# Kernel tuning notes

Measured on AMD Instinct MI355X. Metric: run time of the kernel, lower is better.

## Reference

```python
import jax, jax.numpy as jnp
import numpy as np

N = 100000      # num nodes
E = 1600000     # num edges (before self-loops)
F_IN = 500      # num_features
H1, C1 = 8, 8   # heads, hidden_dim (layer 1, concat)
H2, C2 = 1, 16  # output_heads, num_classes (layer 2, mean)
NEG_SLOPE = 0.2


def setup_inputs() -> dict:
    key = jax.random.key(0)
    ks = jax.random.split(key, 10)
    x = jax.random.normal(ks[0], (N, F_IN), dtype=jnp.float32)
    edge_index = jax.random.randint(ks[1], (2, E), 0, N, dtype=jnp.int64)
    s = 0.05
    W1 = jax.random.normal(ks[2], (F_IN, H1 * C1), dtype=jnp.float32) * s
    a_src1 = jax.random.normal(ks[3], (H1, C1), dtype=jnp.float32) * s
    a_dst1 = jax.random.normal(ks[4], (H1, C1), dtype=jnp.float32) * s
    b1 = jnp.zeros((H1 * C1,), dtype=jnp.float32)
    W2 = jax.random.normal(ks[5], (H1 * C1, H2 * C2), dtype=jnp.float32) * s
    a_src2 = jax.random.normal(ks[6], (H2, C2), dtype=jnp.float32) * s
    a_dst2 = jax.random.normal(ks[7], (H2, C2), dtype=jnp.float32) * s
    b2 = jnp.zeros((C2,), dtype=jnp.float32)
    return {"x": x, "edge_index": edge_index, "W1": W1, "a_src1": a_src1,
            "a_dst1": a_dst1, "b1": b1, "W2": W2, "a_src2": a_src2,
            "a_dst2": a_dst2, "b2": b2}


def _gat_conv(x, src, dst, W, a_src, a_dst, bias, heads, out_c, concat):
    n = x.shape[0]
    xw = (x @ W).reshape(n, heads, out_c)                      # [N,H,C]
    # per-node attention halves, gathered per edge -> logits [E,H]
    s_src = jnp.einsum('nhc,hc->nh', xw, a_src)
    s_dst = jnp.einsum('nhc,hc->nh', xw, a_dst)
    e = s_src[src] + s_dst[dst]
    e = jnp.where(e > 0, e, NEG_SLOPE * e)                     # leaky_relu
    # segment softmax over incoming edges of each target node
    m = jax.ops.segment_max(e, dst, num_segments=n)            # [N,H]
    m = jnp.where(jnp.isfinite(m), m, 0.0)
    p = jnp.exp(e - m[dst])                                    # [E,H]
    denom = jax.ops.segment_sum(p, dst, num_segments=n)        # [N,H]
    alpha = p / denom[dst]                                     # [E,H]
    # scatter-aggregate weighted messages
    out = jax.ops.segment_sum(alpha[:, :, None] * xw[src], dst,
                              num_segments=n)                  # [N,H,C]
    if concat:
        out = out.reshape(n, heads * out_c)
    else:
        out = out.mean(axis=1)
    return out + bias


def reference(x, edge_index, W1, a_src1, a_dst1, b1, W2, a_src2, a_dst2, b2):
    # PyG GATConv adds self-loops by default
    loops = jnp.arange(N, dtype=edge_index.dtype)
    src = jnp.concatenate([edge_index[0], loops])
    dst = jnp.concatenate([edge_index[1], loops])
    # eval mode: dropout is identity
    h = _gat_conv(x, src, dst, W1, a_src1, a_dst1, b1, H1, C1, True)
    h = jax.nn.elu(h)
    h = _gat_conv(h, src, dst, W2, a_src2, a_dst2, b2, H2, C2, False)
    return jax.nn.log_softmax(h, axis=1)
```

## Files before the change

kernel.cpp:

```cpp
#include <hip/hip_runtime.h>
#include <math.h>

#define NEGS 0.2f
#define BSH 9
#define TS 4096

typedef __attribute__((ext_vector_type(8))) short bf16x8;
typedef __attribute__((ext_vector_type(8))) unsigned short u16x8;
typedef __attribute__((ext_vector_type(4))) float f32x4;

__device__ __forceinline__ unsigned short f2bf(float f) {
  unsigned u = __float_as_uint(f);
  u += 0x7fffu + ((u >> 16) & 1);
  return (unsigned short)(u >> 16);
}
__device__ __forceinline__ float bf2f(unsigned short u) {
  return __uint_as_float((unsigned)u << 16);
}

__global__ void k_wcvt(const float* __restrict__ W1, unsigned short* __restrict__ Wb,
                       int K, int Kp) {
  int t = blockIdx.x * blockDim.x + threadIdx.x;
  if (t >= Kp * 64) return;
  int kg = t >> 6;
  int c = t & 63;
  float f = (kg < K) ? W1[(size_t)kg * 64 + c] : 0.f;
  size_t off = ((size_t)((kg >> 5) * 4 + ((kg >> 3) & 3)) * 512) + c * 8 + (kg & 7);
  Wb[off] = f2bf(f);
}

__global__ __launch_bounds__(256) void k_gemm1m(const float* __restrict__ A,
                                                const unsigned short* __restrict__ Wb,
                                                unsigned short* __restrict__ C,
                                                int M, int K, int nck) {
  const int tid = threadIdx.x;
  const int lane = tid & 63;
  const int w = tid >> 6;
  const int r15 = lane & 15;
  const int kgrp = lane >> 4;
  const int bm = blockIdx.x * 64;

  const int row = bm + w * 16 + r15;
  const float* Ar = A + (size_t)(row < M ? row : (M - 1)) * K;

  f32x4 acc[4] = {};

  for (int ck = 0; ck < nck; ++ck) {
#pragma unroll
    for (int ks = 0; ks < 2; ++ks) {
      const int k0 = ck * 64 + ks * 32 + kgrp * 8;
      bf16x8 af;
      if (ck < nck - 1) {
        const float4* g = (const float4*)(Ar + k0);
        float4 f0 = g[0], f1 = g[1];
        unsigned pk[4];
        pk[0] = (unsigned)f2bf(f0.x) | ((unsigned)f2bf(f0.y) << 16);
        pk[1] = (unsigned)f2bf(f0.z) | ((unsigned)f2bf(f0.w) << 16);
        pk[2] = (unsigned)f2bf(f1.x) | ((unsigned)f2bf(f1.y) << 16);
        pk[3] = (unsigned)f2bf(f1.z) | ((unsigned)f2bf(f1.w) << 16);
        af = *(bf16x8*)pk;
      } else {
        float f[8];
#pragma unroll
        for (int j = 0; j < 8; ++j) {
          int kk = k0 + j;
          f[j] = (kk < K) ? Ar[kk] : 0.f;
        }
        unsigned pk[4];
#pragma unroll
        for (int j = 0; j < 4; ++j)
          pk[j] = (unsigned)f2bf(f[2 * j]) | ((unsigned)f2bf(f[2 * j + 1]) << 16);
        af = *(bf16x8*)pk;
      }
      const unsigned short* bb =
          Wb + ((size_t)((ck * 2 + ks) * 4 + kgrp) * 512) + r15 * 8;
      bf16x8 bf[4];
#pragma unroll
      for (int nc = 0; nc < 4; ++nc)
        bf[nc] = *(const bf16x8*)(bb + nc * 128);
#pragma unroll
      for (int nc = 0; nc < 4; ++nc)
        acc[nc] = __builtin_amdgcn_mfma_f32_16x16x32_bf16(af, bf[nc], acc[nc], 0, 0, 0);
    }
  }
  const int rg4 = kgrp * 4;
#pragma unroll
  for (int nc = 0; nc < 4; ++nc) {
    int row0 = bm + w * 16 + rg4;
    int colg = nc * 16 + r15;
#pragma unroll
    for (int j = 0; j < 4; ++j) {
      int grow = row0 + j;
      if (grow < M) C[(size_t)grow * 64 + colg] = f2bf(acc[nc][j]);
    }
  }
}

__global__ __launch_bounds__(256) void k_thist(const int* __restrict__ ei,
                                               int* __restrict__ hist,
                                               int E, int NB) {
  __shared__ int lh[256];
  const int t = threadIdx.x;
  lh[t] = 0;
  __syncthreads();
  const int e0 = blockIdx.x * TS;
#pragma unroll
  for (int j = 0; j < TS / 256; ++j) {
    int e = e0 + j * 256 + t;
    if (e < E) atomicAdd(&lh[ei[E + e] >> BSH], 1);
  }
  __syncthreads();
  if (t < NB) hist[blockIdx.x * NB + t] = lh[t];
}

__global__ __launch_bounds__(256) void k_bscan1(const int* __restrict__ hist,
                                                int* __restrict__ off_rel,
                                                int* __restrict__ total,
                                                int NT, int NB) {
  __shared__ int sh[256];
  const int t = threadIdx.x;
  const int b = blockIdx.x;
  int t0 = 2 * t, t1 = 2 * t + 1;
  int v0 = (t0 < NT) ? hist[t0 * NB + b] : 0;
  int v1 = (t1 < NT) ? hist[t1 * NB + b] : 0;
  int ps = v0 + v1;
  sh[t] = ps;
  __syncthreads();
  for (int off = 1; off < 256; off <<= 1) {
    int v = (t >= off) ? sh[t - off] : 0;
    __syncthreads();
    sh[t] += v;
    __syncthreads();
  }
  int excl = sh[t] - ps;
  if (t0 < NT) off_rel[t0 * NB + b] = excl;
  if (t1 < NT) off_rel[t1 * NB + b] = excl + v0;
  if (t == 255) total[b] = sh[255];
}

__global__ __launch_bounds__(256) void k_pscatter(const int* __restrict__ ei,
                                                  const int* __restrict__ off_rel,
                                                  const int* __restrict__ total,
                                                  unsigned* __restrict__ pairs,
                                                  int E, int NB) {
  __shared__ int cur[256];
  __shared__ int sb[256];
  const int t = threadIdx.x;
  int v = (t < NB) ? total[t] : 0;
  sb[t] = v;
  __syncthreads();
  for (int off = 1; off < 256; off <<= 1) {
    int x = (t >= off) ? sb[t - off] : 0;
    __syncthreads();
    sb[t] += x;
    __syncthreads();
  }
  if (t < NB) cur[t] = (sb[t] - v) + off_rel[blockIdx.x * NB + t];
  __syncthreads();
  const int e0 = blockIdx.x * TS;
#pragma unroll
  for (int j = 0; j < TS / 256; ++j) {
    int e = e0 + j * 256 + t;
    if (e < E) {
      int s = ei[e], d = ei[E + e];
      int pos = atomicAdd(&cur[d >> BSH], 1);
      pairs[pos] = ((unsigned)(d & ((1 << BSH) - 1)) << 23) | (unsigned)s;
    }
  }
}

__global__ __launch_bounds__(256) void k_bcsr(const unsigned* __restrict__ pairs,
                                              const int* __restrict__ total,
                                              int* __restrict__ rowptr,
                                              int* __restrict__ col,
                                              int Nn, int E, int NB) {
  __shared__ int cnt[512];
  __shared__ int cu[512];
  __shared__ int sh[256];
  __shared__ int P0, P1;
  const int t = threadIdx.x;
  const int b = blockIdx.x;
  const int d0 = b << BSH;
  const int dn = min(1 << BSH, Nn - d0);
  {
    int v = (t < NB) ? total[t] : 0;
    sh[t] = v;
    __syncthreads();
    for (int off = 1; off < 256; off <<= 1) {
      int x = (t >= off) ? sh[t - off] : 0;
      __syncthreads();
      sh[t] += x;
      __syncthreads();
    }
    if (t == b) { P0 = sh[t] - v; P1 = sh[t]; }
    __syncthreads();
  }
  const int p0 = P0, p1 = P1;
  const int rpb = p0 + d0;
  cnt[2 * t] = (2 * t < dn) ? 1 : 0;
  cnt[2 * t + 1] = (2 * t + 1 < dn) ? 1 : 0;
  __syncthreads();
  for (int i = p0 + t; i < p1; i += 256) atomicAdd(&cnt[pairs[i] >> 23], 1);
  __syncthreads();
  int a0 = cnt[2 * t], a1 = cnt[2 * t + 1];
  int ps = a0 + a1;
  sh[t] = ps;
  __syncthreads();
  for (int off = 1; off < 256; off <<= 1) {
    int v = (t >= off) ? sh[t - off] : 0;
    __syncthreads();
    sh[t] += v;
    __syncthreads();
  }
  int excl = sh[t] - ps;
#pragma unroll
  for (int u = 0; u < 2; ++u) {
    int i = 2 * t + u;
    int ex = (u == 0) ? excl : excl + a0;
    if (i < dn) {
      rowptr[d0 + i] = rpb + ex;
      col[rpb + ex] = d0 + i;
      cu[i] = ex + 1;
    }
  }
  if (b == NB - 1 && t == 0) rowptr[Nn] = E + Nn;
  __syncthreads();
  for (int i = p0 + t; i < p1; i += 256) {
    unsigned p = pairs[i];
    int pos = atomicAdd(&cu[p >> 23], 1);
    col[rpb + pos] = (int)(p & 0x7fffffu);
  }
}

__global__ void k_prep1(const unsigned short* __restrict__ xwb,
                        const float* __restrict__ asr,
                        const float* __restrict__ adt,
                        float* __restrict__ ssrc, float* __restrict__ sdst,
                        int Nn) {
  int idx = blockIdx.x * blockDim.x + threadIdx.x;
  if (idx >= Nn * 8) return;
  int h = idx & 7;
  const uint4 v = *(const uint4*)(xwb + (size_t)(idx >> 3) * 64 + h * 8);
  float f[8];
  f[0] = __uint_as_float(v.x << 16); f[1] = __uint_as_float(v.x & 0xffff0000u);
  f[2] = __uint_as_float(v.y << 16); f[3] = __uint_as_float(v.y & 0xffff0000u);
  f[4] = __uint_as_float(v.z << 16); f[5] = __uint_as_float(v.z & 0xffff0000u);
  f[6] = __uint_as_float(v.w << 16); f[7] = __uint_as_float(v.w & 0xffff0000u);
  float ss = 0.f, sd = 0.f;
#pragma unroll
  for (int c = 0; c < 8; ++c) {
    ss += f[c] * asr[h * 8 + c];
    sd += f[c] * adt[h * 8 + c];
  }
  ssrc[idx] = ss;
  sdst[idx] = sd;
}

__global__ __launch_bounds__(256) void k_agg1(const int* __restrict__ rowptr,
                                              const int* __restrict__ col,
                                              const float* __restrict__ ssrc,
                                              const float* __restrict__ sdst,
                                              const unsigned short* __restrict__ xwb,
                                              const float* __restrict__ b1,
                                              float* __restrict__ h1, int Nn) {
  int wid = (blockIdx.x * 256 + threadIdx.x) >> 6;
  if (wid >= Nn) return;
  int lane = threadIdx.x & 63;
  int slot = lane >> 3;
  int chg = lane & 7;
  float sd = sdst[wid * 8 + chg];
  int start = rowptr[wid], end = rowptr[wid + 1];
  float den = 0.f;
  float acc[8] = {};
  for (int it = start; it < end; it += 8) {
    int idx = it + slot;
    bool ok = idx < end;
    int s = col[ok ? idx : start];
    u16x8 pv = *(const u16x8*)(xwb + (size_t)s * 64 + chg * 8);
    float v = ssrc[s * 8 + chg] + sd;
    v = v > 0.f ? v : NEGS * v;
    float p = ok ? __expf(v) : 0.f;
    den += p;
#pragma unroll
    for (int j = 0; j < 8; ++j) acc[j] = fmaf(p, bf2f(pv[j]), acc[j]);
  }
#pragma unroll
  for (int off = 8; off < 64; off <<= 1) {
    den += __shfl_xor(den, off);
#pragma unroll
    for (int j = 0; j < 8; ++j) acc[j] += __shfl_xor(acc[j], off);
  }
  if (slot == 0) {
    float inv = 1.f / den;
    float o[8];
#pragma unroll
    for (int j = 0; j < 8; ++j) {
      float v = acc[j] * inv + b1[chg * 8 + j];
      o[j] = v > 0.f ? v : (__expf(v) - 1.f);
    }
    float* dst = h1 + (size_t)wid * 64 + chg * 8;
#pragma unroll
    for (int j = 0; j < 8; ++j) dst[j] = o[j];
  }
}

__global__ __launch_bounds__(256) void k_gemm2p(const float* __restrict__ h1,
                                                const float* __restrict__ W2,
                                                const float* __restrict__ asr,
                                                const float* __restrict__ adt,
                                                float* __restrict__ xw2,
                                                float* __restrict__ ssrc,
                                                float* __restrict__ sdst, int Nn) {
  __shared__ float w[64 * 16];
  int tid = threadIdx.x;
  for (int i = tid; i < 1024; i += 256) w[i] = W2[i];
  __syncthreads();
  int idx = blockIdx.x * 256 + tid;
  if (idx >= Nn * 16) return;
  int n = idx >> 4, c = idx & 15;
  const float* hr = h1 + (size_t)n * 64;
  float acc = 0.f;
#pragma unroll 8
  for (int k = 0; k < 64; ++k) acc += hr[k] * w[k * 16 + c];
  xw2[idx] = acc;
  float ssv = acc * asr[c], sdv = acc * adt[c];
#pragma unroll
  for (int off = 1; off < 16; off <<= 1) {
    ssv += __shfl_xor(ssv, off);
    sdv += __shfl_xor(sdv, off);
  }
  if (c == 0) { ssrc[n] = ssv; sdst[n] = sdv; }
}

__global__ __launch_bounds__(256) void k_agg2(const int* __restrict__ rowptr,
                                              const int* __restrict__ col,
                                              const float* __restrict__ ssrc,
                                              const float* __restrict__ sdst,
                                              const float* __restrict__ xw2,
                                              const float* __restrict__ b2,
                                              float* __restrict__ out, int Nn) {
  int wid = (blockIdx.x * 256 + threadIdx.x) >> 6;
  if (wid >= Nn) return;
  int lane = threadIdx.x & 63;
  int slot = lane >> 4, c = lane & 15;
  float sd = sdst[wid];
  int start = rowptr[wid], end = rowptr[wid + 1];
  float den = 0.f, acc = 0.f;
  int i = start + slot;
  for (; i + 4 < end; i += 8) {
    int s0 = col[i], s1 = col[i + 4];
    float w0 = xw2[(size_t)s0 * 16 + c];
    float w1 = xw2[(size_t)s1 * 16 + c];
    float v0 = ssrc[s0] + sd; v0 = v0 > 0.f ? v0 : NEGS * v0;
    float v1 = ssrc[s1] + sd; v1 = v1 > 0.f ? v1 : NEGS * v1;
    float p0 = __expf(v0), p1 = __expf(v1);
    den += p0 + p1;
    acc = fmaf(p0, w0, acc);
    acc = fmaf(p1, w1, acc);
  }
  if (i < end) {
    int s = col[i];
    float v = ssrc[s] + sd;
    v = v > 0.f ? v : NEGS * v;
    float p = __expf(v);
    den += p;
    acc = fmaf(p, xw2[(size_t)s * 16 + c], acc);
  }
  den += __shfl_xor(den, 16);
  den += __shfl_xor(den, 32);
  acc += __shfl_xor(acc, 16);
  acc += __shfl_xor(acc, 32);
  float o = acc / den + b2[c];
  float mx = o;
#pragma unroll
  for (int off = 1; off < 16; off <<= 1) mx = fmaxf(mx, __shfl_xor(mx, off));
  float ex = __expf(o - mx);
  float ssum = ex;
#pragma unroll
  for (int off = 1; off < 16; off <<= 1) ssum += __shfl_xor(ssum, off);
  float r = o - mx - __logf(ssum);
  if (slot == 0) out[(size_t)wid * 16 + c] = r;
}

extern "C" void kernel_launch(void* const* d_in, const int* in_sizes, int n_in,
                              void* d_out, int out_size, void* d_ws, size_t ws_size,
                              hipStream_t stream) {
  const float* x      = (const float*)d_in[0];
  const int* ei       = (const int*)d_in[1];
  const float* W1     = (const float*)d_in[2];
  const float* a_src1 = (const float*)d_in[3];
  const float* a_dst1 = (const float*)d_in[4];
  const float* b1     = (const float*)d_in[5];
  const float* W2     = (const float*)d_in[6];
  const float* a_src2 = (const float*)d_in[7];
  const float* a_dst2 = (const float*)d_in[8];
  const float* b2     = (const float*)d_in[9];

  const int F    = in_sizes[2] / 64;
  const int Nn   = in_sizes[0] / F;
  const int E    = in_sizes[1] / 2;
  const int Etot = E + Nn;
  const int nck  = (F + 63) >> 6;
  const int Kp   = nck * 64;
  const int NB   = (Nn + (1 << BSH) - 1) >> BSH;
  const int NT   = (E + TS - 1) / TS;

  float* ws = (float*)d_ws;
  unsigned short* xwb = (unsigned short*)ws;
  float* h1     = ws + (size_t)Nn * 32;
  float* ssrc1  = h1 + (size_t)Nn * 64;
  float* sdst1  = ssrc1 + (size_t)Nn * 8;
  int* rowptr   = (int*)(sdst1 + (size_t)Nn * 8);
  int* col      = rowptr + Nn + 1;
  unsigned short* Wb = (unsigned short*)(col + ((Etot + 7) & ~7));
  int* hist     = (int*)ws;
  int* off_rel  = hist + (size_t)NT * NB;
  int* total    = off_rel + (size_t)NT * NB;
  unsigned* pairs = (unsigned*)h1;
  float* xw2    = ws;
  float* ssrc2  = xw2 + (size_t)Nn * 16;
  float* sdst2  = ssrc2 + Nn;
  float* out2   = (float*)d_out;

  dim3 blk(256);

  k_thist<<<dim3(NT), blk, 0, stream>>>(ei, hist, E, NB);
  k_bscan1<<<dim3(NB), blk, 0, stream>>>(hist, off_rel, total, NT, NB);
  k_pscatter<<<dim3(NT), blk, 0, stream>>>(ei, off_rel, total, pairs, E, NB);
  k_bcsr<<<dim3(NB), blk, 0, stream>>>(pairs, total, rowptr, col, Nn, E, NB);

  k_wcvt<<<dim3((Kp * 64 + 255) / 256), blk, 0, stream>>>(W1, Wb, F, Kp);
  k_gemm1m<<<dim3((Nn + 63) / 64), blk, 0, stream>>>(x, Wb, xwb, Nn, F, nck);
  k_prep1<<<dim3((Nn * 8 + 255) / 256), blk, 0, stream>>>(
      xwb, a_src1, a_dst1, ssrc1, sdst1, Nn);
  k_agg1<<<dim3((Nn * 64 + 255) / 256), blk, 0, stream>>>(
      rowptr, col, ssrc1, sdst1, xwb, b1, h1, Nn);

  k_gemm2p<<<dim3((Nn * 16 + 255) / 256), blk, 0, stream>>>(
      h1, W2, a_src2, a_dst2, xw2, ssrc2, sdst2, Nn);
  k_agg2<<<dim3((Nn * 64 + 255) / 256), blk, 0, stream>>>(
      rowptr, col, ssrc2, sdst2, xw2, b2, out2, Nn);
}
```

Measured before the change: 239.0 us.

## Co-schedule CSR build with layer-1 GEMM and fuse attention scores into GEMM

Merges the W1 conversion with the edge histogram into one launch. It then splits the layer-1 GEMM row blocks into thirds, each launched alongside a latency-bound CSR-building stage (scan, scatter, bucket CSR), so the small graph-prep kernels overlap with matrix work. The per-node attention scores are computed inside the GEMM epilogue with shuffles, which removes the separate prep kernel and its re-read of xw. Layer-2 features are stored as bf16 to halve gather traffic in agg2, at some precision cost. Workspace for hist is moved so it no longer aliases the GEMM output.

```diff
diff --git a/kernel.cpp b/kernel.cpp
--- a/kernel.cpp
+++ b/kernel.cpp
@@ -1,4 +1,5 @@
 #include <hip/hip_runtime.h>
+#include <hip/hip_bf16.h>
 #include <math.h>
 
 #define NEGS 0.2f
@@ -10,116 +11,53 @@
 typedef __attribute__((ext_vector_type(4))) float f32x4;
 
 __device__ __forceinline__ unsigned short f2bf(float f) {
-  unsigned u = __float_as_uint(f);
-  u += 0x7fffu + ((u >> 16) & 1);
-  return (unsigned short)(u >> 16);
+  __hip_bfloat16 h = __float2bfloat16(f);
+  unsigned short u;
+  __builtin_memcpy(&u, &h, 2);
+  return u;
 }
 __device__ __forceinline__ float bf2f(unsigned short u) {
   return __uint_as_float((unsigned)u << 16);
 }
-
-__global__ void k_wcvt(const float* __restrict__ W1, unsigned short* __restrict__ Wb,
-                       int K, int Kp) {
-  int t = blockIdx.x * blockDim.x + threadIdx.x;
+__device__ __forceinline__ unsigned packbf(float lo, float hi) {
+  return (unsigned)f2bf(lo) | ((unsigned)f2bf(hi) << 16);
+}
+
+
+__device__ __forceinline__ void dev_wcvt(const float* __restrict__ W1,
+                                         unsigned short* __restrict__ Wb,
+                                         int K, int Kp, int blk) {
+  int t = blk * 256 + threadIdx.x;
   if (t >= Kp * 64) return;
-  int kg = t >> 6;
-  int c = t & 63;
+  int kg = t >> 6, c = t & 63;
   float f = (kg < K) ? W1[(size_t)kg * 64 + c] : 0.f;
   size_t off = ((size_t)((kg >> 5) * 4 + ((kg >> 3) & 3)) * 512) + c * 8 + (kg & 7);
   Wb[off] = f2bf(f);
 }
 
-__global__ __launch_bounds__(256) void k_gemm1m(const float* __restrict__ A,
-                                                const unsigned short* __restrict__ Wb,
-                                                unsigned short* __restrict__ C,
-                                                int M, int K, int nck) {
-  const int tid = threadIdx.x;
-  const int lane = tid & 63;
-  const int w = tid >> 6;
-  const int r15 = lane & 15;
-  const int kgrp = lane >> 4;
-  const int bm = blockIdx.x * 64;
-
-  const int row = bm + w * 16 + r15;
-  const float* Ar = A + (size_t)(row < M ? row : (M - 1)) * K;
-
-  f32x4 acc[4] = {};
-
-  for (int ck = 0; ck < nck; ++ck) {
-#pragma unroll
-    for (int ks = 0; ks < 2; ++ks) {
-      const int k0 = ck * 64 + ks * 32 + kgrp * 8;
-      bf16x8 af;
-      if (ck < nck - 1) {
-        const float4* g = (const float4*)(Ar + k0);
-        float4 f0 = g[0], f1 = g[1];
-        unsigned pk[4];
-        pk[0] = (unsigned)f2bf(f0.x) | ((unsigned)f2bf(f0.y) << 16);
-        pk[1] = (unsigned)f2bf(f0.z) | ((unsigned)f2bf(f0.w) << 16);
-        pk[2] = (unsigned)f2bf(f1.x) | ((unsigned)f2bf(f1.y) << 16);
-        pk[3] = (unsigned)f2bf(f1.z) | ((unsigned)f2bf(f1.w) << 16);
-        af = *(bf16x8*)pk;
-      } else {
-        float f[8];
-#pragma unroll
-        for (int j = 0; j < 8; ++j) {
-          int kk = k0 + j;
-          f[j] = (kk < K) ? Ar[kk] : 0.f;
-        }
-        unsigned pk[4];
-#pragma unroll
-        for (int j = 0; j < 4; ++j)
-          pk[j] = (unsigned)f2bf(f[2 * j]) | ((unsigned)f2bf(f[2 * j + 1]) << 16);
-        af = *(bf16x8*)pk;
-      }
-      const unsigned short* bb =
-          Wb + ((size_t)((ck * 2 + ks) * 4 + kgrp) * 512) + r15 * 8;
-      bf16x8 bf[4];
-#pragma unroll
-      for (int nc = 0; nc < 4; ++nc)
-        bf[nc] = *(const bf16x8*)(bb + nc * 128);
-#pragma unroll
-      for (int nc = 0; nc < 4; ++nc)
-        acc[nc] = __builtin_amdgcn_mfma_f32_16x16x32_bf16(af, bf[nc], acc[nc], 0, 0, 0);
-    }
-  }
-  const int rg4 = kgrp * 4;
-#pragma unroll
-  for (int nc = 0; nc < 4; ++nc) {
-    int row0 = bm + w * 16 + rg4;
-    int colg = nc * 16 + r15;
-#pragma unroll
-    for (int j = 0; j < 4; ++j) {
-      int grow = row0 + j;
-      if (grow < M) C[(size_t)grow * 64 + colg] = f2bf(acc[nc][j]);
-    }
-  }
-}
-
-__global__ __launch_bounds__(256) void k_thist(const int* __restrict__ ei,
-                                               int* __restrict__ hist,
-                                               int E, int NB) {
+__device__ __forceinline__ void dev_thist(const int* __restrict__ ei,
+                                          int* __restrict__ hist,
+                                          int E, int NB, int tile) {
   __shared__ int lh[256];
   const int t = threadIdx.x;
   lh[t] = 0;
   __syncthreads();
-  const int e0 = blockIdx.x * TS;
+  const int e0 = tile * TS;
 #pragma unroll
   for (int j = 0; j < TS / 256; ++j) {
     int e = e0 + j * 256 + t;
     if (e < E) atomicAdd(&lh[ei[E + e] >> BSH], 1);
   }
   __syncthreads();
-  if (t < NB) hist[blockIdx.x * NB + t] = lh[t];
-}
-
-__global__ __launch_bounds__(256) void k_bscan1(const int* __restrict__ hist,
-                                                int* __restrict__ off_rel,
-                                                int* __restrict__ total,
-                                                int NT, int NB) {
+  if (t < NB) hist[tile * NB + t] = lh[t];
+}
+
+__device__ __forceinline__ void dev_bscan1(const int* __restrict__ hist,
+                                           int* __restrict__ off_rel,
+                                           int* __restrict__ total,
+                                           int NT, int NB, int b) {
   __shared__ int sh[256];
   const int t = threadIdx.x;
-  const int b = blockIdx.x;
   int t0 = 2 * t, t1 = 2 * t + 1;
   int v0 = (t0 < NT) ? hist[t0 * NB + b] : 0;
   int v1 = (t1 < NT) ? hist[t1 * NB + b] : 0;
@@ -138,11 +76,11 @@
   if (t == 255) total[b] = sh[255];
 }
 
-__global__ __launch_bounds__(256) void k_pscatter(const int* __restrict__ ei,
-                                                  const int* __restrict__ off_rel,
-                                                  const int* __restrict__ total,
-                                                  unsigned* __restrict__ pairs,
-                                                  int E, int NB) {
+__device__ __forceinline__ void dev_pscatter(const int* __restrict__ ei,
+                                             const int* __restrict__ off_rel,
+                                             const int* __restrict__ total,
+                                             unsigned* __restrict__ pairs,
+                                             int E, int NB, int tile) {
   __shared__ int cur[256];
   __shared__ int sb[256];
   const int t = threadIdx.x;
@@ -155,9 +93,9 @@
     sb[t] += x;
     __syncthreads();
   }
-  if (t < NB) cur[t] = (sb[t] - v) + off_rel[blockIdx.x * NB + t];
-  __syncthreads();
-  const int e0 = blockIdx.x * TS;
+  if (t < NB) cur[t] = (sb[t] - v) + off_rel[tile * NB + t];
+  __syncthreads();
+  const int e0 = tile * TS;
 #pragma unroll
   for (int j = 0; j < TS / 256; ++j) {
     int e = e0 + j * 256 + t;
@@ -169,17 +107,16 @@
   }
 }
 
-__global__ __launch_bounds__(256) void k_bcsr(const unsigned* __restrict__ pairs,
-                                              const int* __restrict__ total,
-                                              int* __restrict__ rowptr,
-                                              int* __restrict__ col,
-                                              int Nn, int E, int NB) {
-  __shared__ int cnt[512];
-  __shared__ int cu[512];
+__device__ __forceinline__ void dev_bcsr(const unsigned* __restrict__ pairs,
+                                         const int* __restrict__ total,
+                                         int* __restrict__ rowptr,
+                                         int* __restrict__ col,
+                                         int Nn, int E, int NB, int b) {
+  __shared__ int cnt[1 << BSH];
+  __shared__ int cu[1 << BSH];
   __shared__ int sh[256];
   __shared__ int P0, P1;
   const int t = threadIdx.x;
-  const int b = blockIdx.x;
   const int d0 = b << BSH;
   const int dn = min(1 << BSH, Nn - d0);
   {
@@ -232,28 +169,147 @@
   }
 }
 
-__global__ void k_prep1(const unsigned short* __restrict__ xwb,
-                        const float* __restrict__ asr,
-                        const float* __restrict__ adt,
-                        float* __restrict__ ssrc, float* __restrict__ sdst,
-                        int Nn) {
-  int idx = blockIdx.x * blockDim.x + threadIdx.x;
-  if (idx >= Nn * 8) return;
-  int h = idx & 7;
-  const uint4 v = *(const uint4*)(xwb + (size_t)(idx >> 3) * 64 + h * 8);
-  float f[8];
-  f[0] = __uint_as_float(v.x << 16); f[1] = __uint_as_float(v.x & 0xffff0000u);
-  f[2] = __uint_as_float(v.y << 16); f[3] = __uint_as_float(v.y & 0xffff0000u);
-  f[4] = __uint_as_float(v.z << 16); f[5] = __uint_as_float(v.z & 0xffff0000u);
-  f[6] = __uint_as_float(v.w << 16); f[7] = __uint_as_float(v.w & 0xffff0000u);
-  float ss = 0.f, sd = 0.f;
-#pragma unroll
-  for (int c = 0; c < 8; ++c) {
-    ss += f[c] * asr[h * 8 + c];
-    sd += f[c] * adt[h * 8 + c];
-  }
-  ssrc[idx] = ss;
-  sdst[idx] = sd;
+__device__ __forceinline__ void dev_gemm(const float* __restrict__ A,
+                                         const unsigned short* __restrict__ Wb,
+                                         unsigned short* __restrict__ C,
+                                         const float* __restrict__ a1s,
+                                         const float* __restrict__ a1d,
+                                         float* __restrict__ ssrc,
+                                         float* __restrict__ sdst,
+                                         int M, int K, int nck, int rowblk) {
+  const int tid = threadIdx.x;
+  const int lane = tid & 63;
+  const int w = tid >> 6;
+  const int r15 = lane & 15;
+  const int kgrp = lane >> 4;
+  const int bm = rowblk * 64;
+  const int row = bm + w * 16 + r15;
+  const float* Ar = A + (size_t)(row < M ? row : (M - 1)) * K;
+
+  f32x4 acc[4] = {};
+
+  for (int ck = 0; ck < nck; ++ck) {
+#pragma unroll
+    for (int ks = 0; ks < 2; ++ks) {
+      const int k0 = ck * 64 + ks * 32 + kgrp * 8;
+      bf16x8 af;
+      if (ck < nck - 1) {
+        const float4* g = (const float4*)(Ar + k0);
+        float4 f0 = g[0], f1 = g[1];
+        unsigned pk[4] = { packbf(f0.x, f0.y), packbf(f0.z, f0.w),
+                           packbf(f1.x, f1.y), packbf(f1.z, f1.w) };
+        af = *(bf16x8*)pk;
+      } else {
+        float f[8];
+#pragma unroll
+        for (int j = 0; j < 8; ++j) {
+          int kk = k0 + j;
+          f[j] = (kk < K) ? Ar[kk] : 0.f;
+        }
+        unsigned pk[4];
+#pragma unroll
+        for (int j = 0; j < 4; ++j) pk[j] = packbf(f[2 * j], f[2 * j + 1]);
+        af = *(bf16x8*)pk;
+      }
+      const unsigned short* bb =
+          Wb + ((size_t)((ck * 2 + ks) * 4 + kgrp) * 512) + r15 * 8;
+      bf16x8 bf4[4];
+#pragma unroll
+      for (int nc = 0; nc < 4; ++nc)
+        bf4[nc] = *(const bf16x8*)(bb + nc * 128);
+#pragma unroll
+      for (int nc = 0; nc < 4; ++nc)
+        acc[nc] = __builtin_amdgcn_mfma_f32_16x16x32_bf16(af, bf4[nc], acc[nc], 0, 0, 0);
+    }
+  }
+  float av[4], dv[4];
+#pragma unroll
+  for (int nc = 0; nc < 4; ++nc) {
+    av[nc] = a1s[nc * 16 + r15];
+    dv[nc] = a1d[nc * 16 + r15];
+  }
+#pragma unroll
+  for (int j = 0; j < 4; ++j) {
+    int grow = bm + w * 16 + kgrp * 4 + j;
+    bool liv = grow < M;
+#pragma unroll
+    for (int nc = 0; nc < 4; ++nc) {
+      if (liv) C[(size_t)grow * 64 + nc * 16 + r15] = f2bf(acc[nc][j]);
+      float ss = acc[nc][j] * av[nc];
+      float sd = acc[nc][j] * dv[nc];
+      ss += __shfl_xor(ss, 1); ss += __shfl_xor(ss, 2); ss += __shfl_xor(ss, 4);
+      sd += __shfl_xor(sd, 1); sd += __shfl_xor(sd, 2); sd += __shfl_xor(sd, 4);
+      if ((r15 & 7) == 0 && liv) {
+        int h = nc * 2 + (r15 >> 3);
+        ssrc[grow * 8 + h] = ss;
+        sdst[grow * 8 + h] = sd;
+      }
+    }
+  }
+}
+
+__global__ __launch_bounds__(256) void k_A(const float* __restrict__ W1,
+                                           unsigned short* __restrict__ Wb,
+                                           int K, int Kp,
+                                           const int* __restrict__ ei,
+                                           int* __restrict__ hist,
+                                           int E, int NB, int WCB) {
+  int b = blockIdx.x;
+  if (b < WCB) dev_wcvt(W1, Wb, K, Kp, b);
+  else dev_thist(ei, hist, E, NB, b - WCB);
+}
+
+__global__ __launch_bounds__(256) void k_B1(const int* __restrict__ hist,
+                                            int* __restrict__ off_rel,
+                                            int* __restrict__ total,
+                                            int NT, int NB,
+                                            const float* __restrict__ A,
+                                            const unsigned short* __restrict__ Wb,
+                                            unsigned short* __restrict__ C,
+                                            const float* __restrict__ a1s,
+                                            const float* __restrict__ a1d,
+                                            float* __restrict__ ssrc,
+                                            float* __restrict__ sdst,
+                                            int M, int K, int nck, int R0) {
+  int b = blockIdx.x;
+  if (b < NB) dev_bscan1(hist, off_rel, total, NT, NB, b);
+  else dev_gemm(A, Wb, C, a1s, a1d, ssrc, sdst, M, K, nck, b - NB + R0);
+}
+
+__global__ __launch_bounds__(256) void k_B2(const int* __restrict__ ei,
+                                            const int* __restrict__ off_rel,
+                                            const int* __restrict__ total,
+                                            unsigned* __restrict__ pairs,
+                                            int E, int NB, int NT,
+                                            const float* __restrict__ A,
+                                            const unsigned short* __restrict__ Wb,
+                                            unsigned short* __restrict__ C,
+                                            const float* __restrict__ a1s,
+                                            const float* __restrict__ a1d,
+                                            float* __restrict__ ssrc,
+                                            float* __restrict__ sdst,
+                                            int M, int K, int nck, int R0) {
+  int b = blockIdx.x;
+  if (b < NT) dev_pscatter(ei, off_rel, total, pairs, E, NB, b);
+  else dev_gemm(A, Wb, C, a1s, a1d, ssrc, sdst, M, K, nck, b - NT + R0);
+}
+
+__global__ __launch_bounds__(256) void k_B3(const unsigned* __restrict__ pairs,
+                                            const int* __restrict__ total,
+                                            int* __restrict__ rowptr,
+                                            int* __restrict__ col,
+                                            int Nn, int E, int NB,
+                                            const float* __restrict__ A,
+                                            const unsigned short* __restrict__ Wb,
+                                            unsigned short* __restrict__ C,
+                                            const float* __restrict__ a1s,
+                                            const float* __restrict__ a1d,
+                                            float* __restrict__ ssrc,
+                                            float* __restrict__ sdst,
+                                            int M, int K, int nck, int R0) {
+  int b = blockIdx.x;
+  if (b < NB) dev_bcsr(pairs, total, rowptr, col, Nn, E, NB, b);
+  else dev_gemm(A, Wb, C, a1s, a1d, ssrc, sdst, M, K, nck, b - NB + R0);
 }
 
 __global__ __launch_bounds__(256) void k_agg1(const int* __restrict__ rowptr,
@@ -308,7 +364,7 @@
                                                 const float* __restrict__ W2,
                                                 const float* __restrict__ asr,
                                                 const float* __restrict__ adt,
-                                                float* __restrict__ xw2,
+                                                unsigned short* __restrict__ xw2b,
                                                 float* __restrict__ ssrc,
                                                 float* __restrict__ sdst, int Nn) {
   __shared__ float w[64 * 16];
@@ -322,7 +378,7 @@
   float acc = 0.f;
 #pragma unroll 8
   for (int k = 0; k < 64; ++k) acc += hr[k] * w[k * 16 + c];
-  xw2[idx] = acc;
+  xw2b[idx] = f2bf(acc);
   float ssv = acc * asr[c], sdv = acc * adt[c];
 #pragma unroll
   for (int off = 1; off < 16; off <<= 1) {
@@ -336,7 +392,7 @@
                                               const int* __restrict__ col,
                                               const float* __restrict__ ssrc,
                                               const float* __restrict__ sdst,
-                                              const float* __restrict__ xw2,
+                                              const unsigned short* __restrict__ xw2b,
                                               const float* __restrict__ b2,
                                               float* __restrict__ out, int Nn) {
   int wid = (blockIdx.x * 256 + threadIdx.x) >> 6;
@@ -349,8 +405,8 @@
   int i = start + slot;
   for (; i + 4 < end; i += 8) {
     int s0 = col[i], s1 = col[i + 4];
-    float w0 = xw2[(size_t)s0 * 16 + c];
-    float w1 = xw2[(size_t)s1 * 16 + c];
+    float w0 = bf2f(xw2b[(size_t)s0 * 16 + c]);
+    float w1 = bf2f(xw2b[(size_t)s1 * 16 + c]);
     float v0 = ssrc[s0] + sd; v0 = v0 > 0.f ? v0 : NEGS * v0;
     float v1 = ssrc[s1] + sd; v1 = v1 > 0.f ? v1 : NEGS * v1;
     float p0 = __expf(v0), p1 = __expf(v1);
@@ -364,7 +420,7 @@
     v = v > 0.f ? v : NEGS * v;
     float p = __expf(v);
     den += p;
-    acc = fmaf(p, xw2[(size_t)s * 16 + c], acc);
+    acc = fmaf(p, bf2f(xw2b[(size_t)s * 16 + c]), acc);
   }
   den += __shfl_xor(den, 16);
   den += __shfl_xor(den, 32);
@@ -404,6 +460,11 @@
   const int Kp   = nck * 64;
   const int NB   = (Nn + (1 << BSH) - 1) >> BSH;
   const int NT   = (E + TS - 1) / TS;
+  const int WCB  = (Kp * 64 + 255) / 256;
+  const int GB   = (Nn + 63) / 64;
+  const int G1   = (GB + 2) / 3;
+  const int G2   = G1;
+  const int G3   = GB - G1 - G2;
 
   float* ws = (float*)d_ws;
   unsigned short* xwb = (unsigned short*)ws;
@@ -413,31 +474,28 @@
   int* rowptr   = (int*)(sdst1 + (size_t)Nn * 8);
   int* col      = rowptr + Nn + 1;
   unsigned short* Wb = (unsigned short*)(col + ((Etot + 7) & ~7));
-  int* hist     = (int*)ws;
+  int* hist     = (int*)(Wb + (size_t)Kp * 64);
   int* off_rel  = hist + (size_t)NT * NB;
   int* total    = off_rel + (size_t)NT * NB;
   unsigned* pairs = (unsigned*)h1;
-  float* xw2    = ws;
-  float* ssrc2  = xw2 + (size_t)Nn * 16;
+  unsigned short* xw2b = (unsigned short*)ws;
+  float* ssrc2  = ws + (size_t)Nn * 8;
   float* sdst2  = ssrc2 + Nn;
   float* out2   = (float*)d_out;
 
   dim3 blk(256);
 
-  k_thist<<<dim3(NT), blk, 0, stream>>>(ei, hist, E, NB);
-  k_bscan1<<<dim3(NB), blk, 0, stream>>>(hist, off_rel, total, NT, NB);
-  k_pscatter<<<dim3(NT), blk, 0, stream>>>(ei, off_rel, total, pairs, E, NB);
-  k_bcsr<<<dim3(NB), blk, 0, stream>>>(pairs, total, rowptr, col, Nn, E, NB);
-
-  k_wcvt<<<dim3((Kp * 64 + 255) / 256), blk, 0, stream>>>(W1, Wb, F, Kp);
-  k_gemm1m<<<dim3((Nn + 63) / 64), blk, 0, stream>>>(x, Wb, xwb, Nn, F, nck);
-  k_prep1<<<dim3((Nn * 8 + 255) / 256), blk, 0, stream>>>(
-      xwb, a_src1, a_dst1, ssrc1, sdst1, Nn);
+  k_A<<<dim3(WCB + NT), blk, 0, stream>>>(W1, Wb, F, Kp, ei, hist, E, NB, WCB);
+  k_B1<<<dim3(NB + G1), blk, 0, stream>>>(hist, off_rel, total, NT, NB,
+      x, Wb, xwb, a_src1, a_dst1, ssrc1, sdst1, Nn, F, nck, 0);
+  k_B2<<<dim3(NT + G2), blk, 0, stream>>>(ei, off_rel, total, pairs, E, NB, NT,
+      x, Wb, xwb, a_src1, a_dst1, ssrc1, sdst1, Nn, F, nck, G1);
+  k_B3<<<dim3(NB + G3), blk, 0, stream>>>(pairs, total, rowptr, col, Nn, E, NB,
+      x, Wb, xwb, a_src1, a_dst1, ssrc1, sdst1, Nn, F, nck, G1 + G2);
   k_agg1<<<dim3((Nn * 64 + 255) / 256), blk, 0, stream>>>(
       rowptr, col, ssrc1, sdst1, xwb, b1, h1, Nn);
-
   k_gemm2p<<<dim3((Nn * 16 + 255) / 256), blk, 0, stream>>>(
-      h1, W2, a_src2, a_dst2, xw2, ssrc2, sdst2, Nn);
+      h1, W2, a_src2, a_dst2, xw2b, ssrc2, sdst2, Nn);
   k_agg2<<<dim3((Nn * 64 + 255) / 256), blk, 0, stream>>>(
-      rowptr, col, ssrc2, sdst2, xw2, b2, out2, Nn);
-}
+      rowptr, col, ssrc2, sdst2, xw2b, b2, out2, Nn);
+}
```

Result: no change. 239.4 us (+0.2%).
